# Kernel optimization log

Hardware: AMD Instinct MI355X
Metric: run time of the kernel (lower is better)

The kernel has to match this reference:

```python
import jax, jax.numpy as jnp
import numpy as np

N = 50000          # nodes
E = 500000         # edges
EMB = 64           # hidden_size
R = 2              # DDE num_rounds
RR = 2             # DDE num_reverse_rounds
PRED_IN = 4 * EMB + 4 + 4 * (R + RR)  # 276


def setup_inputs() -> dict:
    key = jax.random.key(0)
    ks = jax.random.split(key, 10)
    x = jax.random.normal(ks[0], (N, EMB), jnp.float32)
    edge_index = jax.random.randint(ks[1], (2, E), 0, N, dtype=jnp.int64)
    edge_attr = jax.random.normal(ks[2], (E, EMB), jnp.float32)
    topic_signal = jax.random.uniform(ks[3], (N, 2), dtype=jnp.float32)
    q_emb = jax.random.normal(ks[4], (E, EMB), jnp.float32)
    # learned parameters
    non_text_emb = jax.random.normal(ks[5], (1, EMB), jnp.float32)
    W1 = jax.random.normal(ks[6], (PRED_IN, EMB), jnp.float32) / np.sqrt(PRED_IN)
    b1 = jnp.zeros((EMB,), jnp.float32)
    W2 = jax.random.normal(ks[7], (EMB, 1), jnp.float32) / np.sqrt(EMB)
    b2 = jnp.zeros((1,), jnp.float32)
    return dict(x=x, edge_index=edge_index, edge_attr=edge_attr,
                topic_signal=topic_signal, q_emb=q_emb,
                non_text_emb=non_text_emb, W1=W1, b1=b1, W2=W2, b2=b2)


def _segment_mean(data, seg, num_segments):
    # mean aggregation as in PyG MessagePassing(aggr='mean'); empty segments -> 0
    s = jax.ops.segment_sum(data, seg, num_segments=num_segments)
    cnt = jax.ops.segment_sum(jnp.ones((seg.shape[0],), data.dtype), seg,
                              num_segments=num_segments)
    return s / jnp.maximum(cnt, 1.0)[:, None]


def reference(x, edge_index, edge_attr, topic_signal, q_emb,
              non_text_emb, W1, b1, W2, b2):
    src, dst = edge_index[0], edge_index[1]
    # replace all-zero node rows with the learned non-text entity embedding
    zero_mask = jnp.all(x == 0, axis=1)
    x = jnp.where(zero_mask[:, None], non_text_emb[0], x)

    feats = [x, topic_signal]  # topic_pe = True
    # DDE forward rounds: aggregate src -> dst along edge_index
    h = topic_signal
    for _ in range(R):
        h = _segment_mean(h[src], dst, N)
        feats.append(h)
    # DDE reverse rounds: flipped edges (dst -> src)
    h = topic_signal
    for _ in range(RR):
        h = _segment_mean(h[dst], src, N)
        feats.append(h)

    h_e = jnp.concatenate(feats, axis=1)                      # [N, EMB+2+2*(R+RR)]
    h_triple = jnp.concatenate([q_emb, h_e[src], edge_attr, h_e[dst]], axis=1)  # [E, PRED_IN]
    hidden = jax.nn.relu(h_triple @ W1 + b1)                  # [E, EMB]
    return (hidden @ W2 + b2).squeeze(-1)                     # [E]
```

## Files before the change

kernel.cpp:

```cpp
#include <hip/hip_runtime.h>
#include <cstdint>
#include <cstddef>


typedef __bf16 bf16x8 __attribute__((ext_vector_type(8)));
typedef float f32x4 __attribute__((ext_vector_type(4)));

__device__ __forceinline__ unsigned int f2bf1(float f) {
    unsigned int u = __float_as_uint(f);
    return (u + 0x7fffu + ((u >> 16) & 1u)) >> 16;
}
__device__ __forceinline__ unsigned int pk2(float a, float b) {
    return f2bf1(a) | (f2bf1(b) << 16);
}
__device__ __forceinline__ bf16x8 cvt8(const float* __restrict__ p) {
    float4 v0 = *(const float4*)p;
    float4 v1 = *(const float4*)(p + 4);
    bf16x8 r;
    r[0] = (__bf16)v0.x; r[1] = (__bf16)v0.y; r[2] = (__bf16)v0.z; r[3] = (__bf16)v0.w;
    r[4] = (__bf16)v1.x; r[5] = (__bf16)v1.y; r[6] = (__bf16)v1.z; r[7] = (__bf16)v1.w;
    return r;
}


__global__ void k_detect(const int* __restrict__ idx, int E, int* __restrict__ flag) {
    int e = blockIdx.x * blockDim.x + threadIdx.x;
    bool nz = (e < E) && (idx[2 * e + 1] != 0);
    unsigned long long m = __ballot(nz);
    if (m != 0ull && (threadIdx.x & 63) == 0) atomicOr(flag, 1);
}

__global__ void k_convert(const int* __restrict__ idx, int E, const int* __restrict__ flag,
                          int* __restrict__ src_i, int* __restrict__ dst_i,
                          int* __restrict__ cnt_dst, int* __restrict__ cnt_src,
                          unsigned short* __restrict__ pos_f, unsigned short* __restrict__ pos_r) {
    int e = blockIdx.x * blockDim.x + threadIdx.x;
    if (e >= E) return;
    int s, d;
    if (*flag) { s = idx[e];     d = idx[E + e]; }
    else       { s = idx[2 * e]; d = idx[2 * E + 2 * e]; }
    src_i[e] = s; dst_i[e] = d;
    pos_f[e] = (unsigned short)atomicAdd(&cnt_dst[d], 1);
    pos_r[e] = (unsigned short)atomicAdd(&cnt_src[s], 1);
}

__global__ void k_scan(const int* __restrict__ cnt_dst, const int* __restrict__ cnt_src,
                       int* __restrict__ off_f, int* __restrict__ off_r, int N) {
    const int* cnt = (blockIdx.x == 0) ? cnt_dst : cnt_src;
    int* off       = (blockIdx.x == 0) ? off_f   : off_r;
    const int t = threadIdx.x;
    const int C = (N + 1023) / 1024;
    int lo = t * C, hi = lo + C; if (hi > N) hi = N; if (lo > N) lo = N;
    int sum = 0;
    for (int i = lo; i < hi; ++i) sum += cnt[i];
    __shared__ int wsum[16];
    int lane = t & 63, wv = t >> 6;
    int v = sum;
    for (int ofs = 1; ofs < 64; ofs <<= 1) {
        int u = __shfl_up(v, ofs);
        if (lane >= ofs) v += u;
    }
    if (lane == 63) wsum[wv] = v;
    __syncthreads();
    if (wv == 0) {
        int x = (lane < 16) ? wsum[lane] : 0;
        for (int ofs = 1; ofs < 16; ofs <<= 1) {
            int u = __shfl_up(x, ofs);
            if (lane >= ofs) x += u;
        }
        if (lane < 16) wsum[lane] = x;
    }
    __syncthreads();
    int base = (wv > 0 ? wsum[wv - 1] : 0) + (v - sum);
    for (int i = lo; i < hi; ++i) { off[i] = base; base += cnt[i]; }
}

__global__ void k_fill(const int* __restrict__ src_i, const int* __restrict__ dst_i,
                       const unsigned short* __restrict__ pos_f, const unsigned short* __restrict__ pos_r,
                       const int* __restrict__ off_f, const int* __restrict__ off_r,
                       int* __restrict__ csr_f, int* __restrict__ csr_r, int E) {
    int e = blockIdx.x * blockDim.x + threadIdx.x;
    if (e >= E) return;
    int s = src_i[e], d = dst_i[e];
    csr_f[off_f[d] + pos_f[e]] = s;
    csr_r[off_r[s] + pos_r[e]] = d;
}

__global__ void k_round(const int* __restrict__ off_f, const int* __restrict__ csr_f,
                        const int* __restrict__ off_r, const int* __restrict__ csr_r,
                        const float* __restrict__ hf_in,
                        const float* __restrict__ hr_in,
                        float* __restrict__ f_out, float* __restrict__ r_out,
                        int N, int E) {
    int gid = blockIdx.x * blockDim.x + threadIdx.x;
    if (gid >= 2 * N) return;
    const bool rev = gid >= N;
    const int n = rev ? gid - N : gid;
    const int* __restrict__ off = rev ? off_r : off_f;
    const int* __restrict__ csr = rev ? csr_r : csr_f;
    const float2* __restrict__ h = (const float2*)(rev ? hr_in : hf_in);
    float2* __restrict__ o = (float2*)(rev ? r_out : f_out);
    int b = off[n], e = (n + 1 < N) ? off[n + 1] : E;
    float sx = 0.f, sy = 0.f;
    for (int j = b; j < e; ++j) { float2 t = h[csr[j]]; sx += t.x; sy += t.y; }
    float inv = 1.0f / (float)max(e - b, 1);
    o[n] = make_float2(sx * inv, sy * inv);
}

__global__ void k_build(const float* __restrict__ x, const float* __restrict__ topic,
                        const float* __restrict__ nte,
                        const float* __restrict__ f1, const float* __restrict__ f2,
                        const float* __restrict__ r1, const float* __restrict__ r2,
                        unsigned short* __restrict__ he, int N) {
    int n = blockIdx.x * blockDim.x + threadIdx.x;
    if (n >= N) return;
    const float4* xr = (const float4*)(x + (size_t)n * 64);
    float4 v[16];
    bool allz = true;
#pragma unroll
    for (int i = 0; i < 16; ++i) {
        v[i] = xr[i];
        allz = allz && (v[i].x == 0.f && v[i].y == 0.f && v[i].z == 0.f && v[i].w == 0.f);
    }
    const float4* nr = (const float4*)nte;
    unsigned int row[40];
#pragma unroll
    for (int i = 0; i < 16; ++i) {
        float4 s = allz ? nr[i] : v[i];
        row[2 * i]     = pk2(s.x, s.y);
        row[2 * i + 1] = pk2(s.z, s.w);
    }
    row[32] = pk2(topic[2 * n], topic[2 * n + 1]);
    row[33] = pk2(f1[2 * n], f1[2 * n + 1]);
    row[34] = pk2(f2[2 * n], f2[2 * n + 1]);
    row[35] = pk2(r1[2 * n], r1[2 * n + 1]);
    row[36] = pk2(r2[2 * n], r2[2 * n + 1]);
    row[37] = 0u; row[38] = 0u; row[39] = 0u;
    uint4* dst = (uint4*)(he + (size_t)n * 80);
#pragma unroll
    for (int i = 0; i < 10; ++i) dst[i] = ((const uint4*)row)[i];
}

__global__ void k_w1t(const float* __restrict__ W1, unsigned short* __restrict__ W1T) {
    int i = blockIdx.x * blockDim.x + threadIdx.x;
    if (i >= 64 * 288) return;
    int col = i / 288, pk = i - col * 288;
    int k = 0; bool valid = true;
    if (pk < 64)       { k = pk; }
    else if (pk < 128) { k = 138 + (pk - 64); }
    else if (pk < 208) { int j = pk - 128; k = 64 + j;  valid = j < 74; }
    else               { int j = pk - 208; k = 202 + j; valid = j < 74; }
    float v = valid ? W1[k * 64 + col] : 0.f;
    W1T[col * 288 + pk] = (unsigned short)f2bf1(v);
}


__launch_bounds__(256, 4)
__global__ void k_gemm(const float* __restrict__ q_emb,
                       const float* __restrict__ edge_attr,
                       const unsigned short* __restrict__ he,
                       const unsigned short* __restrict__ W1T,
                       const int* __restrict__ src_i, const int* __restrict__ dst_i,
                       const float* __restrict__ b1, const float* __restrict__ W2,
                       const float* __restrict__ b2, float* __restrict__ out, int E)
{
    const int tid = threadIdx.x;
    const int w = tid >> 6, l = tid & 63, c = l & 15, q = l >> 4;
    const int ebase = blockIdx.x * 128 + w * 32;

    const float* gq[2];
    const float* ga[2];
    const unsigned short* hs[2];
    const unsigned short* hd[2];
#pragma unroll
    for (int t = 0; t < 2; ++t) {
        int ee = ebase + t * 16 + c; ee = ee < E ? ee : E - 1;
        int s = src_i[ee], d = dst_i[ee];
        gq[t] = q_emb     + (size_t)ee * 64 + q * 8;
        ga[t] = edge_attr + (size_t)ee * 64 + q * 8;
        hs[t] = he + (size_t)s * 80 + q * 8;
        hd[t] = he + (size_t)d * 80 + q * 8;
    }

    float b1v[4], w2v[4];
#pragma unroll
    for (int ct = 0; ct < 4; ++ct) { b1v[ct] = b1[ct * 16 + c]; w2v[ct] = W2[ct * 16 + c]; }
    const float bb = b2[0];

    f32x4 acc[2][4] = {};

    const unsigned short* wrow = W1T + (size_t)c * 288 + q * 8;
#define BF(ct, ks) (*(const bf16x8*)(wrow + (ct) * (16 * 288) + (ks) * 32))
#define KSTEP(ks, AEXPR)                                                               \
    {                                                                                  \
        bf16x8 bf0 = BF(0, ks), bf1 = BF(1, ks), bf2 = BF(2, ks), bf3 = BF(3, ks);     \
        _Pragma("unroll")                                                              \
        for (int t = 0; t < 2; ++t) {                                                  \
            bf16x8 a = (AEXPR);                                                        \
            acc[t][0] = __builtin_amdgcn_mfma_f32_16x16x32_bf16(a, bf0, acc[t][0], 0, 0, 0); \
            acc[t][1] = __builtin_amdgcn_mfma_f32_16x16x32_bf16(a, bf1, acc[t][1], 0, 0, 0); \
            acc[t][2] = __builtin_amdgcn_mfma_f32_16x16x32_bf16(a, bf2, acc[t][2], 0, 0, 0); \
            acc[t][3] = __builtin_amdgcn_mfma_f32_16x16x32_bf16(a, bf3, acc[t][3], 0, 0, 0); \
        }                                                                              \
    }

    KSTEP(0, cvt8(gq[t]))
    KSTEP(1, cvt8(gq[t] + 32))
    KSTEP(2, cvt8(ga[t]))
    KSTEP(3, cvt8(ga[t] + 32))
    KSTEP(4, (*(const bf16x8*)(hs[t])))
    KSTEP(5, (*(const bf16x8*)(hs[t] + 32)))
    KSTEP(6, (*(const bf16x8*)((q < 2) ? (hs[t] + 64) : (hd[t] - 16))))
    KSTEP(7, (*(const bf16x8*)(hd[t] + 16)))
    KSTEP(8, (*(const bf16x8*)(hd[t] + 48)))
#undef KSTEP
#undef BF

#pragma unroll
    for (int t = 0; t < 2; ++t) {
        float pr[4];
#pragma unroll
        for (int r = 0; r < 4; ++r) {
            float h0 = fmaxf(acc[t][0][r] + b1v[0], 0.f);
            float h1 = fmaxf(acc[t][1][r] + b1v[1], 0.f);
            float h2 = fmaxf(acc[t][2][r] + b1v[2], 0.f);
            float h3 = fmaxf(acc[t][3][r] + b1v[3], 0.f);
            float p = fmaf(h0, w2v[0], fmaf(h1, w2v[1], fmaf(h2, w2v[2], h3 * w2v[3])));
            p += __shfl_xor(p, 1);
            p += __shfl_xor(p, 2);
            p += __shfl_xor(p, 4);
            p += __shfl_xor(p, 8);
            pr[r] = p;
        }
        if (c == 0) {
            int eo = ebase + t * 16 + q * 4;
            if (eo < E) {
                float4 o = make_float4(pr[0] + bb, pr[1] + bb, pr[2] + bb, pr[3] + bb);
                *(float4*)&out[eo] = o;
            }
        }
    }
}


extern "C" void kernel_launch(void* const* d_in, const int* in_sizes, int n_in,
                              void* d_out, int out_size, void* d_ws, size_t ws_size,
                              hipStream_t stream)
{
    const float* x         = (const float*)d_in[0];
    const int*   eidx      = (const int*)  d_in[1];
    const float* edge_attr = (const float*)d_in[2];
    const float* topic     = (const float*)d_in[3];
    const float* q_emb     = (const float*)d_in[4];
    const float* nte       = (const float*)d_in[5];
    const float* W1        = (const float*)d_in[6];
    const float* b1        = (const float*)d_in[7];
    const float* W2        = (const float*)d_in[8];
    const float* b2        = (const float*)d_in[9];
    float* out = (float*)d_out;

    const int E = out_size;
    const int N = in_sizes[0] / 64;

    char* ws = (char*)d_ws;
    int* flag  = (int*)ws;
    int* src_i = (int*)(ws + 16);
    int* dst_i = src_i + E;
    int* off_f = dst_i + E;
    int* off_r = off_f + N;
    float* fblk = (float*)(off_r + N);
    float* f1 = fblk;
    float* f2 = fblk + 2 * (size_t)N;
    float* r1 = fblk + 4 * (size_t)N;
    float* r2 = fblk + 6 * (size_t)N;
    int* cnt_dst = (int*)f1;
    int* cnt_src = cnt_dst + N;
    char* heblk = (char*)(fblk + 8 * (size_t)N);
    unsigned short* pos_f = (unsigned short*)heblk;
    unsigned short* pos_r = pos_f + E;
    int* csr_f = (int*)(pos_r + E);
    int* csr_r = csr_f + E;
    unsigned short* he = (unsigned short*)heblk;
    size_t he_bytes = (size_t)N * 160;
    size_t trans_bytes = (size_t)E * 12;
    size_t heblk_bytes = he_bytes > trans_bytes ? he_bytes : trans_bytes;
    unsigned short* W1T = (unsigned short*)(heblk + heblk_bytes);

    size_t needed = 16 + (size_t)8 * E + (size_t)8 * N + (size_t)32 * N + heblk_bytes + 64 * 288 * 2;
    if (ws_size < needed) return;

    hipMemsetAsync(flag, 0, 16, stream);
    hipMemsetAsync(cnt_dst, 0, (size_t)8 * N, stream);

    const int gE = (E + 255) / 256;
    const int gN = (N + 255) / 256;
    const int gN2 = (2 * N + 255) / 256;

    k_detect <<<gE, 256, 0, stream>>>(eidx, E, flag);
    k_convert<<<gE, 256, 0, stream>>>(eidx, E, flag, src_i, dst_i,
                                      cnt_dst, cnt_src, pos_f, pos_r);
    k_scan   <<<2, 1024, 0, stream>>>(cnt_dst, cnt_src, off_f, off_r, N);
    k_fill   <<<gE, 256, 0, stream>>>(src_i, dst_i, pos_f, pos_r, off_f, off_r,
                                      csr_f, csr_r, E);
    k_round  <<<gN2, 256, 0, stream>>>(off_f, csr_f, off_r, csr_r, topic, topic, f1, r1, N, E);
    k_round  <<<gN2, 256, 0, stream>>>(off_f, csr_f, off_r, csr_r, f1, r1, f2, r2, N, E);
    k_build  <<<gN, 256, 0, stream>>>(x, topic, nte, f1, f2, r1, r2, he, N);
    k_w1t    <<<(64 * 288 + 255) / 256, 256, 0, stream>>>(W1, W1T);

    k_gemm<<<(E + 127) / 128, 256, 0, stream>>>(q_emb, edge_attr, he, W1T,
                                                src_i, dst_i, b1, W2, b2, out, E);
}
```

Baseline: 601.9 us.

## Make edge GEMM persistent with LDS-staged weights and double-buffered gathers

The edge MLP kernel becomes a persistent grid of 512 blocks of two waves, each wave looping over 16-edge tiles. W1T is loaded once per block into LDS via global_load_lds, so the per-block global re-reads of the weights go away. Node-feature gathers go into double-buffered LDS, and q_emb/edge_attr rows are register-prefetched one tile ahead, with manual vmcnt waits to overlap memory with MFMA. It drops the E tail handling because it assumes E is divisible by 16. The hand-counted waitcnt is fragile, and the smaller grid may reduce occupancy.

```diff
diff --git a/kernel.cpp b/kernel.cpp
--- a/kernel.cpp
+++ b/kernel.cpp
@@ -13,14 +13,17 @@
 __device__ __forceinline__ unsigned int pk2(float a, float b) {
     return f2bf1(a) | (f2bf1(b) << 16);
 }
-__device__ __forceinline__ bf16x8 cvt8(const float* __restrict__ p) {
-    float4 v0 = *(const float4*)p;
-    float4 v1 = *(const float4*)(p + 4);
+__device__ __forceinline__ bf16x8 cvt8v(float4 a, float4 b) {
     bf16x8 r;
-    r[0] = (__bf16)v0.x; r[1] = (__bf16)v0.y; r[2] = (__bf16)v0.z; r[3] = (__bf16)v0.w;
-    r[4] = (__bf16)v1.x; r[5] = (__bf16)v1.y; r[6] = (__bf16)v1.z; r[7] = (__bf16)v1.w;
+    r[0] = (__bf16)a.x; r[1] = (__bf16)a.y; r[2] = (__bf16)a.z; r[3] = (__bf16)a.w;
+    r[4] = (__bf16)b.x; r[5] = (__bf16)b.y; r[6] = (__bf16)b.z; r[7] = (__bf16)b.w;
     return r;
 }
+
+#define GL16(gp, lp)                                                        \
+    __builtin_amdgcn_global_load_lds(                                       \
+        (const __attribute__((address_space(1))) void*)(gp),                \
+        (__attribute__((address_space(3))) void*)(lp), 16, 0, 0)
 
 
 __global__ void k_detect(const int* __restrict__ idx, int E, int* __restrict__ flag) {
@@ -155,76 +158,125 @@
 }
 
 
-__launch_bounds__(256, 4)
+__launch_bounds__(128, 2)
 __global__ void k_gemm(const float* __restrict__ q_emb,
                        const float* __restrict__ edge_attr,
                        const unsigned short* __restrict__ he,
-                       const unsigned short* __restrict__ W1T,
+                       const unsigned short* __restrict__ W1Tg,
                        const int* __restrict__ src_i, const int* __restrict__ dst_i,
                        const float* __restrict__ b1, const float* __restrict__ W2,
                        const float* __restrict__ b2, float* __restrict__ out, int E)
 {
+    __shared__ __align__(64) char smem[57344];
     const int tid = threadIdx.x;
     const int w = tid >> 6, l = tid & 63, c = l & 15, q = l >> 4;
-    const int ebase = blockIdx.x * 128 + w * 32;
-
-    const float* gq[2];
-    const float* ga[2];
-    const unsigned short* hs[2];
-    const unsigned short* hd[2];
-#pragma unroll
-    for (int t = 0; t < 2; ++t) {
-        int ee = ebase + t * 16 + c; ee = ee < E ? ee : E - 1;
-        int s = src_i[ee], d = dst_i[ee];
-        gq[t] = q_emb     + (size_t)ee * 64 + q * 8;
-        ga[t] = edge_attr + (size_t)ee * 64 + q * 8;
-        hs[t] = he + (size_t)s * 80 + q * 8;
-        hd[t] = he + (size_t)d * 80 + q * 8;
-    }
-
+    const int NW = gridDim.x * 2;
+    const int gw = blockIdx.x * 2 + w;
+    const int ntiles = E / 16;
+
+#pragma unroll
+    for (int jj = 0; jj < 18; ++jj) {
+        int j = w * 18 + jj;
+        GL16((const char*)W1Tg + j * 1024 + l * 16, smem + j * 1024);
+    }
+
+    char* buf0 = smem + 36864 + (w * 2) * 5120;
+    char* buf1 = buf0 + 5120;
+
+    int T = gw;
+    {
+        int e0 = T * 16 + (l & 15);
+        int s0 = src_i[e0], d0 = dst_i[e0];
+#pragma unroll
+        for (int j = 0; j < 5; ++j) {
+            int ch = j * 4 + (l >> 4);
+            int node = ch < 10 ? s0 : d0;
+            int chunk = ch < 10 ? ch : ch - 10;
+            GL16((const char*)he + (size_t)node * 160 + chunk * 16, buf0 + j * 1024);
+        }
+    }
+    const float* qr0 = q_emb     + (size_t)(T * 16 + c) * 64 + q * 8;
+    const float* ar0 = edge_attr + (size_t)(T * 16 + c) * 64 + q * 8;
+    float4 qc0 = *(const float4*)qr0,        qc1 = *(const float4*)(qr0 + 4);
+    float4 qc2 = *(const float4*)(qr0 + 32), qc3 = *(const float4*)(qr0 + 36);
+    float4 ec0 = *(const float4*)ar0,        ec1 = *(const float4*)(ar0 + 4);
+    float4 ec2 = *(const float4*)(ar0 + 32), ec3 = *(const float4*)(ar0 + 36);
+    int si_n, di_n;
+    {
+        int en = min(T + NW, ntiles - 1) * 16 + (l & 15);
+        si_n = src_i[en]; di_n = dst_i[en];
+    }
     float b1v[4], w2v[4];
 #pragma unroll
     for (int ct = 0; ct < 4; ++ct) { b1v[ct] = b1[ct * 16 + c]; w2v[ct] = W2[ct * 16 + c]; }
     const float bb = b2[0];
-
-    f32x4 acc[2][4] = {};
-
-    const unsigned short* wrow = W1T + (size_t)c * 288 + q * 8;
-#define BF(ct, ks) (*(const bf16x8*)(wrow + (ct) * (16 * 288) + (ks) * 32))
-#define KSTEP(ks, AEXPR)                                                               \
-    {                                                                                  \
-        bf16x8 bf0 = BF(0, ks), bf1 = BF(1, ks), bf2 = BF(2, ks), bf3 = BF(3, ks);     \
-        _Pragma("unroll")                                                              \
-        for (int t = 0; t < 2; ++t) {                                                  \
-            bf16x8 a = (AEXPR);                                                        \
-            acc[t][0] = __builtin_amdgcn_mfma_f32_16x16x32_bf16(a, bf0, acc[t][0], 0, 0, 0); \
-            acc[t][1] = __builtin_amdgcn_mfma_f32_16x16x32_bf16(a, bf1, acc[t][1], 0, 0, 0); \
-            acc[t][2] = __builtin_amdgcn_mfma_f32_16x16x32_bf16(a, bf2, acc[t][2], 0, 0, 0); \
-            acc[t][3] = __builtin_amdgcn_mfma_f32_16x16x32_bf16(a, bf3, acc[t][3], 0, 0, 0); \
-        }                                                                              \
-    }
-
-    KSTEP(0, cvt8(gq[t]))
-    KSTEP(1, cvt8(gq[t] + 32))
-    KSTEP(2, cvt8(ga[t]))
-    KSTEP(3, cvt8(ga[t] + 32))
-    KSTEP(4, (*(const bf16x8*)(hs[t])))
-    KSTEP(5, (*(const bf16x8*)(hs[t] + 32)))
-    KSTEP(6, (*(const bf16x8*)((q < 2) ? (hs[t] + 64) : (hd[t] - 16))))
-    KSTEP(7, (*(const bf16x8*)(hd[t] + 16)))
-    KSTEP(8, (*(const bf16x8*)(hd[t] + 48)))
-#undef KSTEP
+    __syncthreads();
+
+    int cur = 0;
+    while (T < ntiles) {
+        const int Tn = T + NW;
+        const bool more = Tn < ntiles;
+        float4 qn0, qn1, qn2, qn3, en0, en1, en2, en3;
+        int si_f = si_n, di_f = di_n;
+        char* sbuf = cur ? buf0 : buf1;
+        char* cbuf = cur ? buf1 : buf0;
+
+        if (more) {
+            const float* qr = q_emb     + (size_t)(Tn * 16 + c) * 64 + q * 8;
+            const float* ar = edge_attr + (size_t)(Tn * 16 + c) * 64 + q * 8;
+            qn0 = *(const float4*)qr;        qn1 = *(const float4*)(qr + 4);
+            qn2 = *(const float4*)(qr + 32); qn3 = *(const float4*)(qr + 36);
+            en0 = *(const float4*)ar;        en1 = *(const float4*)(ar + 4);
+            en2 = *(const float4*)(ar + 32); en3 = *(const float4*)(ar + 36);
+#pragma unroll
+            for (int j = 0; j < 5; ++j) {
+                int ch = j * 4 + (l >> 4);
+                int node = ch < 10 ? si_n : di_n;
+                int chunk = ch < 10 ? ch : ch - 10;
+                GL16((const char*)he + (size_t)node * 160 + chunk * 16, sbuf + j * 1024);
+            }
+            int ef = min(Tn + NW, ntiles - 1) * 16 + (l & 15);
+            si_f = src_i[ef]; di_f = dst_i[ef];
+            asm volatile("s_waitcnt vmcnt(15)" ::: "memory");
+        } else {
+            qn0 = qc0; qn1 = qc1; qn2 = qc2; qn3 = qc3;
+            en0 = ec0; en1 = ec1; en2 = ec2; en3 = ec3;
+            asm volatile("s_waitcnt vmcnt(0)" ::: "memory");
+        }
+        __builtin_amdgcn_sched_barrier(0);
+
+        f32x4 acc0 = {}, acc1 = {}, acc2 = {}, acc3 = {};
+        const char* wrow = smem + c * 576 + q * 16;
+#define BF(ct, ks) (*(const bf16x8*)(wrow + (ct) * 9216 + (ks) * 64))
+#define HEF(pl) (*(const bf16x8*)(cbuf + (pl) * 256 + c * 16))
+#define KST(ks, A)                                                                 \
+        {                                                                          \
+            bf16x8 a_ = (A);                                                       \
+            acc0 = __builtin_amdgcn_mfma_f32_16x16x32_bf16(a_, BF(0, ks), acc0, 0, 0, 0); \
+            acc1 = __builtin_amdgcn_mfma_f32_16x16x32_bf16(a_, BF(1, ks), acc1, 0, 0, 0); \
+            acc2 = __builtin_amdgcn_mfma_f32_16x16x32_bf16(a_, BF(2, ks), acc2, 0, 0, 0); \
+            acc3 = __builtin_amdgcn_mfma_f32_16x16x32_bf16(a_, BF(3, ks), acc3, 0, 0, 0); \
+        }
+        KST(0, cvt8v(qc0, qc1))
+        KST(1, cvt8v(qc2, qc3))
+        KST(2, cvt8v(ec0, ec1))
+        KST(3, cvt8v(ec2, ec3))
+        KST(4, HEF(q))
+        KST(5, HEF(q + 4))
+        KST(6, HEF(q + 8))
+        KST(7, HEF(q + 12))
+        KST(8, HEF(q + 16))
+#undef KST
+#undef HEF
 #undef BF
 
-#pragma unroll
-    for (int t = 0; t < 2; ++t) {
         float pr[4];
 #pragma unroll
         for (int r = 0; r < 4; ++r) {
-            float h0 = fmaxf(acc[t][0][r] + b1v[0], 0.f);
-            float h1 = fmaxf(acc[t][1][r] + b1v[1], 0.f);
-            float h2 = fmaxf(acc[t][2][r] + b1v[2], 0.f);
-            float h3 = fmaxf(acc[t][3][r] + b1v[3], 0.f);
+            float h0 = fmaxf(acc0[r] + b1v[0], 0.f);
+            float h1 = fmaxf(acc1[r] + b1v[1], 0.f);
+            float h2 = fmaxf(acc2[r] + b1v[2], 0.f);
+            float h3 = fmaxf(acc3[r] + b1v[3], 0.f);
             float p = fmaf(h0, w2v[0], fmaf(h1, w2v[1], fmaf(h2, w2v[2], h3 * w2v[3])));
             p += __shfl_xor(p, 1);
             p += __shfl_xor(p, 2);
@@ -233,12 +285,14 @@
             pr[r] = p;
         }
         if (c == 0) {
-            int eo = ebase + t * 16 + q * 4;
-            if (eo < E) {
-                float4 o = make_float4(pr[0] + bb, pr[1] + bb, pr[2] + bb, pr[3] + bb);
-                *(float4*)&out[eo] = o;
-            }
-        }
+            *(float4*)&out[T * 16 + q * 4] =
+                make_float4(pr[0] + bb, pr[1] + bb, pr[2] + bb, pr[3] + bb);
+        }
+
+        qc0 = qn0; qc1 = qn1; qc2 = qn2; qc3 = qn3;
+        ec0 = en0; ec1 = en1; ec2 = en2; ec3 = en3;
+        si_n = si_f; di_n = di_f;
+        T = Tn; cur ^= 1;
     }
 }
 
@@ -307,6 +361,6 @@
     k_build  <<<gN, 256, 0, stream>>>(x, topic, nte, f1, f2, r1, r2, he, N);
     k_w1t    <<<(64 * 288 + 255) / 256, 256, 0, stream>>>(W1, W1T);
 
-    k_gemm<<<(E + 127) / 128, 256, 0, stream>>>(q_emb, edge_attr, he, W1T,
-                                                src_i, dst_i, b1, W2, b2, out, E);
-}
+    k_gemm<<<512, 128, 0, stream>>>(q_emb, edge_attr, he, W1T,
+                                    src_i, dst_i, b1, W2, b2, out, E);
+}
```

After: 559.1 us. 7.1% less time.
